# Kernel tuning notes

Measured on AMD Instinct MI355X. Metric: run time of the kernel, lower is better.

The kernel has to match this reference:

```python
import jax, jax.numpy as jnp
import numpy as np

N_HEADS = 16
N_KV_HEADS = 4
HEAD_DIM = 128


def setup_inputs() -> dict:
    key = jax.random.key(0)
    ks = jax.random.split(key, 5)
    B, T, C = 4, 2048, 2048
    kv_dim = N_KV_HEADS * HEAD_DIM
    s = 0.02
    return {
        "x": jax.random.normal(ks[0], (B, T, C), jnp.float32),
        "Wq": jax.random.normal(ks[1], (C, C), jnp.float32) * s,
        "Wk": jax.random.normal(ks[2], (kv_dim, C), jnp.float32) * s,
        "Wv": jax.random.normal(ks[3], (kv_dim, C), jnp.float32) * s,
        "Wo": jax.random.normal(ks[4], (C, C), jnp.float32) * s,
    }


def reference(x, Wq, Wk, Wv, Wo):
    B, T, C = x.shape
    n_rep = N_HEADS // N_KV_HEADS
    # projections (nn.Linear: y = x @ W^T), reshape to (B, H, T, D)
    q = (x @ Wq.T).reshape(B, T, N_HEADS, HEAD_DIM).transpose(0, 2, 1, 3)
    k = (x @ Wk.T).reshape(B, T, N_KV_HEADS, HEAD_DIM).transpose(0, 2, 1, 3)
    v = (x @ Wv.T).reshape(B, T, N_KV_HEADS, HEAD_DIM).transpose(0, 2, 1, 3)
    # GQA: expand kv heads (repeat_interleave on head dim)
    k = jnp.repeat(k, n_rep, axis=1)
    v = jnp.repeat(v, n_rep, axis=1)
    scale = 1.0 / np.sqrt(HEAD_DIM).astype(np.float32)
    scores = jnp.einsum("bhqd,bhkd->bhqk", q, k) * scale
    causal = jnp.tril(jnp.ones((T, T), bool))
    scores = jnp.where(causal[None, None], scores, -jnp.inf)
    attn = jax.nn.softmax(scores, axis=-1)  # dropout p=0 -> identity
    out = jnp.einsum("bhqk,bhkd->bhqd", attn, v)
    out = out.transpose(0, 2, 1, 3).reshape(B, T, C)
    return out @ Wo.T
```

## Files before the change

kernel.cpp:

```cpp
#include <hip/hip_runtime.h>

#define TB 4
#define TT 2048
#define TC 2048
#define NH 16
#define NKV 4
#define HD 128
#define KVDIM (NKV*HD)
#define NQKV (TC + 2*KVDIM)
#define MTOK (TB*TT)

typedef __bf16 bf16x8 __attribute__((ext_vector_type(8)));
typedef __bf16 bf16x2 __attribute__((ext_vector_type(2)));
typedef float  f32x4  __attribute__((ext_vector_type(4)));
typedef float  f32x16 __attribute__((ext_vector_type(16)));
typedef unsigned short ushort_t;
typedef unsigned short us8 __attribute__((ext_vector_type(8)));
typedef unsigned short us4 __attribute__((ext_vector_type(4)));
typedef unsigned int u32x4 __attribute__((ext_vector_type(4)));
typedef unsigned int u32x2 __attribute__((ext_vector_type(2)));

#define QSC 0.12751743f

__device__ __forceinline__ ushort_t f2bf(float f) {
    unsigned u = __builtin_bit_cast(unsigned, f);
    u += 0x7fffu + ((u >> 16) & 1u);
    return (ushort_t)(u >> 16);
}

__device__ __forceinline__ unsigned pkbf(float lo, float hi) {
    bf16x2 v;
    v[0] = (__bf16)lo; v[1] = (__bf16)hi;
    return __builtin_bit_cast(unsigned, v);
}

__device__ __forceinline__ void gload16(const ushort_t* g, ushort_t* l) {
    __builtin_amdgcn_global_load_lds(
        (const __attribute__((address_space(1))) unsigned int*)g,
        (__attribute__((address_space(3))) unsigned int*)l, 16, 0, 0);
}

__global__ __launch_bounds__(256) void cast_all(const float* __restrict__ x,
                                                const float* __restrict__ Wq,
                                                const float* __restrict__ Wk,
                                                const float* __restrict__ Wv,
                                                const float* __restrict__ Wo,
                                                ushort_t* __restrict__ dst) {
    const long E0 = 16777216;
    const long E1 = 20971520;
    const long E2 = 22020096;
    const long E3 = 23068672;
    const long E4 = 27262976;
    long i = (long)blockIdx.x * blockDim.x + threadIdx.x;
    long stride = (long)gridDim.x * blockDim.x;
    for (long e = i * 4; e < E4; e += stride * 4) {
        const float* src; long off;
        if (e < E0)      { src = x;  off = e; }
        else if (e < E1) { src = Wq; off = e - E0; }
        else if (e < E2) { src = Wk; off = e - E1; }
        else if (e < E3) { src = Wv; off = e - E2; }
        else             { src = Wo; off = e - E3; }
        float4 v = *reinterpret_cast<const float4*>(src + off);
        us4 o;
        o[0] = f2bf(v.x); o[1] = f2bf(v.y); o[2] = f2bf(v.z); o[3] = f2bf(v.w);
        *reinterpret_cast<us4*>(dst + e) = o;
    }
}

#define LBLK 8192

template<bool OUTF32, bool QSCALE>
__global__ __launch_bounds__(512, 2) void gemm256(const ushort_t* __restrict__ A,
                                                  const ushort_t* __restrict__ Bw,
                                                  float* __restrict__ Cf,
                                                  ushort_t* __restrict__ Cb,
                                                  int Nld, int Kd, int nbn) {
    extern __shared__ ushort_t lds[];
    const int tid = threadIdx.x;
    const int lane = tid & 63, wid = tid >> 6;
    const int wm = wid >> 2, wn = wid & 3;
    const int g = lane >> 4, l16 = lane & 15;

    const int cpx = gridDim.x >> 3;
    const int swz = (blockIdx.x & 7) * cpx + (blockIdx.x >> 3);
    const int bm = swz / nbn, bn = swz % nbn;

    const ushort_t* Ag = A  + (size_t)bm * 256 * Kd;
    const ushort_t* Bg = Bw + (size_t)bn * 256 * Kd;

    const int r0 = tid >> 3;
    const int p0 = (tid & 7) ^ (r0 & 7);
    const size_t so0 = (size_t)r0 * Kd + p0 * 8;
    const size_t so1 = so0 + (size_t)64 * Kd;
    const int ldsw0 = wid * 512;

    f32x4 acc[8][4] = {};
    bf16x8 aA[4][2], bB[2][2];

    const int NK = Kd >> 6;
    const int NI = Kd >> 7;

#define STAGE(mat, half, tile) do { if ((tile) < NK) {                                   \
    const ushort_t* sg_ = ((mat) ? Bg : Ag) + (size_t)(half) * 128 * Kd + (size_t)(tile) * 64; \
    ushort_t* lb_ = lds + (((((tile)&1)*2 + (mat))*2 + (half)) * LBLK) + ldsw0;          \
    gload16(sg_ + so0, lb_);                                                             \
    gload16(sg_ + so1, lb_ + 4096);                                                      \
} } while(0)

#define LDA(buf, qm) do {                                                                \
    const ushort_t* Ah_ = lds + (((buf)*2 + 0)*2 + wm) * LBLK;                           \
    _Pragma("unroll") for (int mi_ = 0; mi_ < 4; mi_++) {                                \
        const int r_ = (qm)*64 + mi_*16 + l16;                                           \
        _Pragma("unroll") for (int ks_ = 0; ks_ < 2; ks_++)                              \
            aA[mi_][ks_] = *reinterpret_cast<const bf16x8*>(                             \
                Ah_ + r_*64 + (((ks_*4 + g) ^ (r_ & 7)) * 8));                           \
    }                                                                                    \
} while(0)

#define LDB(buf, qn) do {                                                                \
    const ushort_t* Bh_ = lds + (((buf)*2 + 1)*2 + (wn >> 1)) * LBLK;                    \
    _Pragma("unroll") for (int nj_ = 0; nj_ < 2; nj_++) {                                \
        const int r_ = (wn & 1)*64 + (qn)*32 + nj_*16 + l16;                             \
        _Pragma("unroll") for (int ks_ = 0; ks_ < 2; ks_++)                              \
            bB[nj_][ks_] = *reinterpret_cast<const bf16x8*>(                             \
                Bh_ + r_*64 + (((ks_*4 + g) ^ (r_ & 7)) * 8));                           \
    }                                                                                    \
} while(0)

#define MM(qm, qn) do {                                                                  \
    __builtin_amdgcn_s_setprio(1);                                                       \
    _Pragma("unroll") for (int mi_ = 0; mi_ < 4; mi_++)                                  \
    _Pragma("unroll") for (int nj_ = 0; nj_ < 2; nj_++)                                  \
    _Pragma("unroll") for (int ks_ = 0; ks_ < 2; ks_++)                                  \
        acc[(qm)*4 + mi_][(qn)*2 + nj_] = __builtin_amdgcn_mfma_f32_16x16x32_bf16(       \
            aA[mi_][ks_], bB[nj_][ks_], acc[(qm)*4 + mi_][(qn)*2 + nj_], 0, 0, 0);       \
    __builtin_amdgcn_s_setprio(0);                                                       \
} while(0)

#define PH_MID() do {                                                                    \
    __builtin_amdgcn_s_barrier();                                                        \
    asm volatile("s_waitcnt lgkmcnt(0)" ::: "memory");                                   \
    __builtin_amdgcn_sched_barrier(0);                                                   \
} while(0)

#define PH_END() __builtin_amdgcn_s_barrier()
#define PH_END_VM4() do { asm volatile("s_waitcnt vmcnt(4)" ::: "memory");               \
                          __builtin_amdgcn_s_barrier(); } while(0)
#define PH_END_VM0() do { asm volatile("s_waitcnt vmcnt(0)" ::: "memory");               \
                          __builtin_amdgcn_s_barrier(); } while(0)

    STAGE(0, 0, 0); STAGE(0, 1, 0); STAGE(1, 0, 0); STAGE(1, 1, 0);
    STAGE(0, 0, 1); STAGE(0, 1, 1);
    asm volatile("s_waitcnt vmcnt(4)" ::: "memory");
    __builtin_amdgcn_s_barrier();

    for (int i = 0; i < NI; ++i) {
        const int t0 = 2 * i, t1 = 2 * i + 1;
        const bool last = (i == NI - 1);
        LDA(0, 0); LDB(0, 0);
        STAGE(1, 0, t1); STAGE(1, 1, t1);
        PH_MID(); MM(0, 0); PH_END();
        LDB(0, 1);
        PH_MID(); MM(0, 1); PH_END();
        LDA(0, 1); LDB(0, 0);
        PH_MID(); MM(1, 0); PH_END();
        LDB(0, 1);
        STAGE(0, 0, t0 + 2); STAGE(0, 1, t0 + 2);
        PH_MID(); MM(1, 1);
        if (last) PH_END_VM0(); else PH_END_VM4();
        LDA(1, 0); LDB(1, 0);
        STAGE(1, 0, t0 + 2); STAGE(1, 1, t0 + 2);
        PH_MID(); MM(0, 0); PH_END();
        LDB(1, 1);
        PH_MID(); MM(0, 1); PH_END();
        LDA(1, 1); LDB(1, 0);
        PH_MID(); MM(1, 0); PH_END();
        LDB(1, 1);
        STAGE(0, 0, t1 + 2); STAGE(0, 1, t1 + 2);
        PH_MID(); MM(1, 1);
        if (last) PH_END_VM0(); else PH_END_VM4();
    }

#pragma unroll
    for (int mi = 0; mi < 8; mi++)
#pragma unroll
        for (int nj = 0; nj < 4; nj++) {
            const int rbase = bm * 256 + wm * 128 + mi * 16 + g * 4;
            const int col   = bn * 256 + wn * 64 + nj * 16 + l16;
#pragma unroll
            for (int r = 0; r < 4; r++) {
                float v = acc[mi][nj][r];
                if (QSCALE) v *= QSC;
                size_t off = (size_t)(rbase + r) * Nld + col;
                if (OUTF32) Cf[off] = v;
                else        Cb[off] = __builtin_bit_cast(ushort_t, (__bf16)v);
            }
        }
#undef STAGE
#undef LDA
#undef LDB
#undef MM
#undef PH_MID
#undef PH_END
#undef PH_END_VM4
#undef PH_END_VM0
}

__global__ __launch_bounds__(512, 2) void gemm_bk32(const ushort_t* __restrict__ A,
                                                    const ushort_t* __restrict__ Bw,
                                                    ushort_t* __restrict__ Cb,
                                                    int Nld, int Kd, int nbn) {
    extern __shared__ ushort_t lds[];
    const int tid = threadIdx.x;
    const int lane = tid & 63, wid = tid >> 6;
    const int wm = wid >> 2, wn = wid & 3;
    const int g = lane >> 4, l16 = lane & 15;

    const int cpx = gridDim.x >> 3;
    const int swz = (blockIdx.x & 7) * cpx + (blockIdx.x >> 3);
    const int bm = swz / nbn, bn = swz % nbn;

    const ushort_t* Ag = A  + (size_t)bm * 128 * Kd;
    const ushort_t* Bg = Bw + (size_t)bn * 256 * Kd;

    const int arow = tid >> 2;
    const int apos = (tid & 3) ^ (arow & 3);
    const size_t aso  = (size_t)arow * Kd + apos * 8;
    const size_t bso0 = aso;
    const size_t bso1 = aso + (size_t)128 * Kd;
    const int ldsw = wid * 512;

    f32x4 acc[4][4] = {};
    bf16x8 aA[4], bB[4];
    const int NK = Kd >> 5;

#define STG(tile, bb) do { if ((tile) < NK) {                                            \
    const ushort_t* a_ = Ag + (size_t)(tile) * 32;                                       \
    const ushort_t* b_ = Bg + (size_t)(tile) * 32;                                       \
    ushort_t* lb_ = lds + (bb) * 12288 + ldsw;                                           \
    gload16(a_ + aso,  lb_);                                                             \
    gload16(b_ + bso0, lb_ + 4096);                                                      \
    gload16(b_ + bso1, lb_ + 8192);                                                      \
} } while(0)

#define LDAB(bb) do {                                                                    \
    const ushort_t* Ah_ = lds + (bb) * 12288;                                            \
    const ushort_t* Bh_ = Ah_ + 4096;                                                    \
    _Pragma("unroll") for (int mi_ = 0; mi_ < 4; mi_++) {                                \
        const int r_ = wm * 64 + mi_ * 16 + l16;                                         \
        aA[mi_] = *reinterpret_cast<const bf16x8*>(Ah_ + r_ * 32 + ((g ^ (r_ & 3)) * 8));\
    }                                                                                    \
    _Pragma("unroll") for (int nj_ = 0; nj_ < 4; nj_++) {                                \
        const int r_ = wn * 64 + nj_ * 16 + l16;                                         \
        bB[nj_] = *reinterpret_cast<const bf16x8*>(Bh_ + r_ * 32 + ((g ^ (r_ & 3)) * 8));\
    }                                                                                    \
} while(0)

    STG(0, 0); STG(1, 1);
    asm volatile("s_waitcnt vmcnt(3)" ::: "memory");
    __builtin_amdgcn_s_barrier();

    int cb = 0;
    for (int t = 0; t < NK; ++t) {
        const int sb = (cb == 0) ? 2 : cb - 1;
        STG(t + 2, sb);
        LDAB(cb);
        asm volatile("s_waitcnt lgkmcnt(0)" ::: "memory");
        __builtin_amdgcn_sched_barrier(0);
        __builtin_amdgcn_s_setprio(1);
#pragma unroll
        for (int mi = 0; mi < 4; mi++)
#pragma unroll
            for (int nj = 0; nj < 4; nj++)
                acc[mi][nj] = __builtin_amdgcn_mfma_f32_16x16x32_bf16(
                    aA[mi], bB[nj], acc[mi][nj], 0, 0, 0);
        __builtin_amdgcn_s_setprio(0);
        if (t + 2 < NK) asm volatile("s_waitcnt vmcnt(3)" ::: "memory");
        else            asm volatile("s_waitcnt vmcnt(0)" ::: "memory");
        __builtin_amdgcn_s_barrier();
        cb = (cb == 2) ? 0 : cb + 1;
    }

#pragma unroll
    for (int mi = 0; mi < 4; mi++)
#pragma unroll
        for (int nj = 0; nj < 4; nj++) {
            const int rbase = bm * 128 + wm * 64 + mi * 16 + g * 4;
            const int col   = bn * 256 + wn * 64 + nj * 16 + l16;
#pragma unroll
            for (int r = 0; r < 4; r++)
                Cb[(size_t)(rbase + r) * Nld + col] =
                    __builtin_bit_cast(ushort_t, (__bf16)acc[mi][nj][r]);
        }
#undef STG
#undef LDAB
}

#define AQB 128
#define AKB 64
#define NTB (TT/AQB)
#define VTS 72

__global__ __launch_bounds__(256, 2) void attn_kernel(const ushort_t* __restrict__ qkv,
                                                      ushort_t* __restrict__ aout) {
    __shared__ alignas(16) ushort_t Ks[2][AKB * HD];
    __shared__ alignas(16) ushort_t Vt[2][HD * VTS];

    const int tid  = threadIdx.x;
    const int lane = tid & 63, wid = tid >> 6;
    const int hi   = lane >> 5, l31 = lane & 31;
    const int gx   = blockIdx.x;
    const int h    = blockIdx.y;
    const int b    = blockIdx.z;
    const int hk   = h >> 2;
    const size_t rowbase = (size_t)b * TT;

    const ushort_t* kg = qkv + TC + hk * HD;
    const ushort_t* vg = qkv + TC + KVDIM + hk * HD;
    const int rswz = (l31 & 7) << 3;

    us8 sk0, sk1, sk2, sk3;
    unsigned vv2[16];
    const int kr = tid >> 2, dcK = (tid & 3) * 32;
    const int vs = ((lane >> 2) & 7) << 3;

    for (int phase = 0; phase < 2; ++phase) {
        const int qb = (phase == 0 ? (NTB - 1 - gx) : gx) * AQB;
        const int q0 = qb + wid * 32;
        const int qrow = q0 + l31;

        bf16x8 qfr[8];
        {
            const ushort_t* qp = qkv + (rowbase + qrow) * NQKV + h * HD + hi * 8;
#pragma unroll
            for (int s = 0; s < 8; s++)
                qfr[s] = *reinterpret_cast<const bf16x8*>(qp + s * 16);
        }

        f32x16 oacc[4];
#pragma unroll
        for (int d = 0; d < 4; d++)
#pragma unroll
            for (int r = 0; r < 16; r++) oacc[d][r] = 0.f;
        float lsum = 0.f;

        const int ntiles = qb / AKB + 2;

        {
            const ushort_t* ksrc = kg + (rowbase + kr) * NQKV + dcK;
            sk0 = *reinterpret_cast<const us8*>(ksrc);
            sk1 = *reinterpret_cast<const us8*>(ksrc + 8);
            sk2 = *reinterpret_cast<const us8*>(ksrc + 16);
            sk3 = *reinterpret_cast<const us8*>(ksrc + 24);
            const ushort_t* vsrc = vg + (rowbase + wid * 16) * NQKV + 2 * lane;
#pragma unroll
            for (int j = 0; j < 16; j++)
                vv2[j] = *reinterpret_cast<const unsigned*>(vsrc + (size_t)j * NQKV);
        }
        if (phase) __syncthreads();

        for (int t = 0; t < ntiles; ++t) {
            const int kp0 = t * AKB;
            const int cur = t & 1;
            {
                const int kb = kr * HD + dcK, ksw = (kr & 7) << 3;
                *reinterpret_cast<us8*>(&Ks[cur][(kb     ) ^ ksw]) = sk0;
                *reinterpret_cast<us8*>(&Ks[cur][(kb +  8) ^ ksw]) = sk1;
                *reinterpret_cast<us8*>(&Ks[cur][(kb + 16) ^ ksw]) = sk2;
                *reinterpret_cast<us8*>(&Ks[cur][(kb + 24) ^ ksw]) = sk3;
                u32x4 pl0, ph0, pl1, ph1;
#pragma unroll
                for (int k = 0; k < 4; k++) {
                    pl0[k] = __builtin_amdgcn_perm(vv2[2 * k + 1], vv2[2 * k], 0x05040100u);
                    ph0[k] = __builtin_amdgcn_perm(vv2[2 * k + 1], vv2[2 * k], 0x07060302u);
                    pl1[k] = __builtin_amdgcn_perm(vv2[8 + 2 * k + 1], vv2[8 + 2 * k], 0x05040100u);
                    ph1[k] = __builtin_amdgcn_perm(vv2[8 + 2 * k + 1], vv2[8 + 2 * k], 0x07060302u);
                }
                ushort_t* r0p = &Vt[cur][(2 * lane) * VTS];
                ushort_t* r1p = &Vt[cur][(2 * lane + 1) * VTS];
                const int o0 = (wid * 16) ^ vs, o1 = (wid * 16 + 8) ^ vs;
                *reinterpret_cast<u32x4*>(r0p + o0) = pl0;
                *reinterpret_cast<u32x4*>(r0p + o1) = pl1;
                *reinterpret_cast<u32x4*>(r1p + o0) = ph0;
                *reinterpret_cast<u32x4*>(r1p + o1) = ph1;
            }
            if (t + 1 < ntiles) {
                const int kn = (t + 1) * AKB;
                const ushort_t* ksrc = kg + (rowbase + kn + kr) * NQKV + dcK;
                sk0 = *reinterpret_cast<const us8*>(ksrc);
                sk1 = *reinterpret_cast<const us8*>(ksrc + 8);
                sk2 = *reinterpret_cast<const us8*>(ksrc + 16);
                sk3 = *reinterpret_cast<const us8*>(ksrc + 24);
                const ushort_t* vsrc = vg + (rowbase + kn + wid * 16) * NQKV + 2 * lane;
#pragma unroll
                for (int j = 0; j < 16; j++)
                    vv2[j] = *reinterpret_cast<const unsigned*>(vsrc + (size_t)j * NQKV);
            }
            __syncthreads();

            if (kp0 <= q0 + 31) {
                f32x16 s0, s1;
#pragma unroll
                for (int r = 0; r < 16; r++) { s0[r] = 0.f; s1[r] = 0.f; }
                __builtin_amdgcn_s_setprio(1);
#pragma unroll
                for (int ds = 0; ds < 8; ds++) {
                    bf16x8 ka = *reinterpret_cast<const bf16x8*>(
                        &Ks[cur][(l31 * HD + ds * 16 + hi * 8) ^ rswz]);
                    s0 = __builtin_amdgcn_mfma_f32_32x32x16_bf16(ka, qfr[ds], s0, 0, 0, 0);
                }
#pragma unroll
                for (int ds = 0; ds < 8; ds++) {
                    bf16x8 ka = *reinterpret_cast<const bf16x8*>(
                        &Ks[cur][((32 + l31) * HD + ds * 16 + hi * 8) ^ rswz]);
                    s1 = __builtin_amdgcn_mfma_f32_32x32x16_bf16(ka, qfr[ds], s1, 0, 0, 0);
                }
                __builtin_amdgcn_s_setprio(0);
                if (kp0 + 63 > q0) {
#pragma unroll
                    for (int r = 0; r < 16; r++) {
                        int k0i = kp0 + (r & 3) + 8 * (r >> 2) + 4 * hi;
                        if (k0i > qrow)      s0[r] = -1e30f;
                        if (k0i + 32 > qrow) s1[r] = -1e30f;
                    }
                }
                unsigned pk0[8], pk1[8];
                float ps = 0.f;
#pragma unroll
                for (int w = 0; w < 8; w++) {
                    float a0 = exp2f(s0[2 * w]), a1 = exp2f(s0[2 * w + 1]);
                    float b0 = exp2f(s1[2 * w]), b1 = exp2f(s1[2 * w + 1]);
                    ps += (a0 + a1) + (b0 + b1);
                    pk0[w] = pkbf(a0, a1);
                    pk1[w] = pkbf(b0, b1);
                }
                ps += __shfl_xor(ps, 32);
                lsum += ps;
                __builtin_amdgcn_s_setprio(1);
#pragma unroll
                for (int ks = 0; ks < 4; ks++) {
                    const unsigned* pkt = (ks < 2) ? pk0 : pk1;
                    unsigned c00 = pkt[4 * (ks & 1) + 0];
                    unsigned c01 = pkt[4 * (ks & 1) + 1];
                    unsigned c10 = pkt[4 * (ks & 1) + 2];
                    unsigned c11 = pkt[4 * (ks & 1) + 3];
                    u32x2 rA = __builtin_amdgcn_permlane32_swap(c00, c10, false, false);
                    u32x2 rB = __builtin_amdgcn_permlane32_swap(c01, c11, false, false);
                    u32x4 faw;
                    faw[0] = rA[0];
                    faw[1] = rB[0];
                    faw[2] = rA[1];
                    faw[3] = rB[1];
                    bf16x8 pa = __builtin_bit_cast(bf16x8, faw);
#pragma unroll
                    for (int dt = 0; dt < 4; dt++) {
                        int doff = dt * 32 + l31;
                        int sr = ((doff >> 3) & 7) << 3;
                        bf16x8 vb = *reinterpret_cast<const bf16x8*>(
                            &Vt[cur][doff * VTS + ((ks * 16 + hi * 8) ^ sr)]);
                        oacc[dt] = __builtin_amdgcn_mfma_f32_32x32x16_bf16(vb, pa, oacc[dt], 0, 0, 0);
                    }
                }
                __builtin_amdgcn_s_setprio(0);
            }
        }

        const float rl = 1.f / lsum;
        ushort_t* orow = aout + (rowbase + qrow) * TC + h * HD;
#pragma unroll
        for (int dt = 0; dt < 4; dt++)
#pragma unroll
            for (int rp = 0; rp < 8; rp++) {
                int d = dt * 32 + ((2 * rp) & 3) + 8 * ((2 * rp) >> 2) + 4 * hi;
                unsigned w = pkbf(oacc[dt][2 * rp] * rl, oacc[dt][2 * rp + 1] * rl);
                *reinterpret_cast<unsigned*>(orow + d) = w;
            }
    }
}

extern "C" void kernel_launch(void* const* d_in, const int* in_sizes, int n_in,
                              void* d_out, int out_size, void* d_ws, size_t ws_size,
                              hipStream_t stream) {
    const float* x  = (const float*)d_in[0];
    const float* Wq = (const float*)d_in[1];
    const float* Wk = (const float*)d_in[2];
    const float* Wv = (const float*)d_in[3];
    const float* Wo = (const float*)d_in[4];
    float* out = (float*)d_out;

    ushort_t* x_bf  = (ushort_t*)d_ws;
    ushort_t* wqkv  = x_bf  + (size_t)MTOK * TC;
    ushort_t* wo_bf = wqkv  + (size_t)NQKV * TC;
    ushort_t* qkv   = wo_bf + (size_t)TC * TC;
    ushort_t* attn  = x_bf;

    cast_all<<<4096, 256, 0, stream>>>(x, Wq, Wk, Wv, Wo, x_bf);

    const int GK_LDS   = 73728;
    const int G256_LDS = 131072;
    hipFuncSetAttribute(reinterpret_cast<const void*>(gemm_bk32),
                        hipFuncAttributeMaxDynamicSharedMemorySize, GK_LDS);
    hipFuncSetAttribute(reinterpret_cast<const void*>(gemm256<false, true>),
                        hipFuncAttributeMaxDynamicSharedMemorySize, G256_LDS);
    hipFuncSetAttribute(reinterpret_cast<const void*>(gemm256<true, false>),
                        hipFuncAttributeMaxDynamicSharedMemorySize, G256_LDS);

    gemm256<false, true><<<dim3(256), 512, G256_LDS, stream>>>(
        x_bf, wqkv, nullptr, qkv, NQKV, TC, 8);

    gemm_bk32<<<dim3(256), 512, GK_LDS, stream>>>(
        x_bf, wqkv + (size_t)TC * TC, qkv + TC, NQKV, TC, 4);

    attn_kernel<<<dim3(NTB / 2, NH, TB), 256, 0, stream>>>(qkv, attn);

    gemm256<true, false><<<dim3(256), 512, G256_LDS, stream>>>(
        attn, wo_bf, out, nullptr, TC, TC, 8);
}
```

Measured before the change: 319.6 us.

## Double attention query block to 256 rows with 512-thread blocks

Grows the attention query tile from 128 to 256 rows and the block from 4 to 8 waves. Each K/V tile staged in shared memory is then reused by twice as many query rows, which halves the global K/V traffic per query. The K and V staging loads and transposes are redistributed so each thread moves half as much data. The trade-offs are half as many blocks (fewer in flight on the GPU), coarser causal load balance, and more register pressure under launch_bounds(512,2).

```diff
diff --git a/kernel.cpp b/kernel.cpp
--- a/kernel.cpp
+++ b/kernel.cpp
@@ -296,12 +296,12 @@
 #undef LDAB
 }
 
-#define AQB 128
+#define AQB 256
 #define AKB 64
 #define NTB (TT/AQB)
 #define VTS 72
 
-__global__ __launch_bounds__(256, 2) void attn_kernel(const ushort_t* __restrict__ qkv,
+__global__ __launch_bounds__(512, 2) void attn_kernel(const ushort_t* __restrict__ qkv,
                                                       ushort_t* __restrict__ aout) {
     __shared__ alignas(16) ushort_t Ks[2][AKB * HD];
     __shared__ alignas(16) ushort_t Vt[2][HD * VTS];
@@ -319,10 +319,13 @@
     const ushort_t* vg = qkv + TC + KVDIM + hk * HD;
     const int rswz = (l31 & 7) << 3;
 
-    us8 sk0, sk1, sk2, sk3;
-    unsigned vv2[16];
-    const int kr = tid >> 2, dcK = (tid & 3) * 32;
-    const int vs = ((lane >> 2) & 7) << 3;
+    us8 sk0, sk1;
+    const int kr = tid >> 3, dcK = (tid & 7) * 16;
+    const int ksw = (kr & 7) << 3;
+    const int kb0 = kr * HD + dcK;
+    unsigned vv[8];
+    const int vd2 = lane * 2;
+    const int vso = ((wid ^ ((lane >> 2) & 7)) * 8);
 
     for (int phase = 0; phase < 2; ++phase) {
         const int qb = (phase == 0 ? (NTB - 1 - gx) : gx) * AQB;
@@ -344,18 +347,16 @@
             for (int r = 0; r < 16; r++) oacc[d][r] = 0.f;
         float lsum = 0.f;
 
-        const int ntiles = qb / AKB + 2;
+        const int ntiles = (qb >> 6) + 4;
 
         {
             const ushort_t* ksrc = kg + (rowbase + kr) * NQKV + dcK;
             sk0 = *reinterpret_cast<const us8*>(ksrc);
             sk1 = *reinterpret_cast<const us8*>(ksrc + 8);
-            sk2 = *reinterpret_cast<const us8*>(ksrc + 16);
-            sk3 = *reinterpret_cast<const us8*>(ksrc + 24);
-            const ushort_t* vsrc = vg + (rowbase + wid * 16) * NQKV + 2 * lane;
-#pragma unroll
-            for (int j = 0; j < 16; j++)
-                vv2[j] = *reinterpret_cast<const unsigned*>(vsrc + (size_t)j * NQKV);
+            const ushort_t* vsrc = vg + (rowbase + wid * 8) * NQKV + vd2;
+#pragma unroll
+            for (int j = 0; j < 8; j++)
+                vv[j] = *reinterpret_cast<const unsigned*>(vsrc + (size_t)j * NQKV);
         }
         if (phase) __syncthreads();
 
@@ -363,38 +364,26 @@
             const int kp0 = t * AKB;
             const int cur = t & 1;
             {
-                const int kb = kr * HD + dcK, ksw = (kr & 7) << 3;
-                *reinterpret_cast<us8*>(&Ks[cur][(kb     ) ^ ksw]) = sk0;
-                *reinterpret_cast<us8*>(&Ks[cur][(kb +  8) ^ ksw]) = sk1;
-                *reinterpret_cast<us8*>(&Ks[cur][(kb + 16) ^ ksw]) = sk2;
-                *reinterpret_cast<us8*>(&Ks[cur][(kb + 24) ^ ksw]) = sk3;
-                u32x4 pl0, ph0, pl1, ph1;
+                *reinterpret_cast<us8*>(&Ks[cur][(kb0    ) ^ ksw]) = sk0;
+                *reinterpret_cast<us8*>(&Ks[cur][(kb0 + 8) ^ ksw]) = sk1;
+                u32x4 plo, phi;
 #pragma unroll
                 for (int k = 0; k < 4; k++) {
-                    pl0[k] = __builtin_amdgcn_perm(vv2[2 * k + 1], vv2[2 * k], 0x05040100u);
-                    ph0[k] = __builtin_amdgcn_perm(vv2[2 * k + 1], vv2[2 * k], 0x07060302u);
-                    pl1[k] = __builtin_amdgcn_perm(vv2[8 + 2 * k + 1], vv2[8 + 2 * k], 0x05040100u);
-                    ph1[k] = __builtin_amdgcn_perm(vv2[8 + 2 * k + 1], vv2[8 + 2 * k], 0x07060302u);
+                    plo[k] = __builtin_amdgcn_perm(vv[2 * k + 1], vv[2 * k], 0x05040100u);
+                    phi[k] = __builtin_amdgcn_perm(vv[2 * k + 1], vv[2 * k], 0x07060302u);
                 }
-                ushort_t* r0p = &Vt[cur][(2 * lane) * VTS];
-                ushort_t* r1p = &Vt[cur][(2 * lane + 1) * VTS];
-                const int o0 = (wid * 16) ^ vs, o1 = (wid * 16 + 8) ^ vs;
-                *reinterpret_cast<u32x4*>(r0p + o0) = pl0;
-                *reinterpret_cast<u32x4*>(r0p + o1) = pl1;
-                *reinterpret_cast<u32x4*>(r1p + o0) = ph0;
-                *reinterpret_cast<u32x4*>(r1p + o1) = ph1;
+                *reinterpret_cast<u32x4*>(&Vt[cur][(vd2    ) * VTS + vso]) = plo;
+                *reinterpret_cast<u32x4*>(&Vt[cur][(vd2 + 1) * VTS + vso]) = phi;
             }
             if (t + 1 < ntiles) {
                 const int kn = (t + 1) * AKB;
                 const ushort_t* ksrc = kg + (rowbase + kn + kr) * NQKV + dcK;
                 sk0 = *reinterpret_cast<const us8*>(ksrc);
                 sk1 = *reinterpret_cast<const us8*>(ksrc + 8);
-                sk2 = *reinterpret_cast<const us8*>(ksrc + 16);
-                sk3 = *reinterpret_cast<const us8*>(ksrc + 24);
-                const ushort_t* vsrc = vg + (rowbase + kn + wid * 16) * NQKV + 2 * lane;
-#pragma unroll
-                for (int j = 0; j < 16; j++)
-                    vv2[j] = *reinterpret_cast<const unsigned*>(vsrc + (size_t)j * NQKV);
+                const ushort_t* vsrc = vg + (rowbase + kn + wid * 8) * NQKV + vd2;
+#pragma unroll
+                for (int j = 0; j < 8; j++)
+                    vv[j] = *reinterpret_cast<const unsigned*>(vsrc + (size_t)j * NQKV);
             }
             __syncthreads();
 
@@ -511,7 +500,7 @@
     gemm_bk32<<<dim3(256), 512, GK_LDS, stream>>>(
         x_bf, wqkv + (size_t)TC * TC, qkv + TC, NQKV, TC, 4);
 
-    attn_kernel<<<dim3(NTB / 2, NH, TB), 256, 0, stream>>>(qkv, attn);
+    attn_kernel<<<dim3(NTB / 2, NH, TB), 512, 0, stream>>>(qkv, attn);
 
     gemm256<true, false><<<dim3(256), 512, G256_LDS, stream>>>(
         attn, wo_bf, out, nullptr, TC, TC, 8);
```

Result: faster. 306.3 us, median of 2 (-4.2%).
